# Kernel tuning notes

Measured on AMD Instinct MI355X. Metric: run time of the kernel, lower is better.

The kernel has to match this reference:

```python
import jax, jax.numpy as jnp
import numpy as np

N = 50000
H = 8          # heads
C = 10         # out channels per head
F_IN = 128
NEG_SLOPE = 0.2


def _glorot(key, shape, fan_in):
    return jax.random.normal(key, shape, dtype=jnp.float32) / np.sqrt(fan_in)


def setup_inputs() -> dict:
    key = jax.random.key(0)
    ks = jax.random.split(key, 16)
    x = jax.random.normal(ks[0], (N, F_IN), dtype=jnp.float32)
    edge_index = jax.random.randint(ks[1], (2, 1600000), 0, N, dtype=jnp.int64)
    inp = {"x": x, "edge_index": edge_index}
    dims = [F_IN, H * C, H * C]  # input dim of each of the 3 layers
    k = 2
    for i, din in enumerate(dims):
        inp[f"Wl{i}"] = _glorot(ks[k + 0], (din, H * C), din)
        inp[f"Wr{i}"] = _glorot(ks[k + 1], (din, H * C), din)
        inp[f"att{i}"] = _glorot(ks[k + 2], (H, C), C)
        inp[f"b{i}"] = jnp.zeros((H * C,), dtype=jnp.float32)
        k += 3
    return inp


def gatv2_layer(x, Wl, Wr, att, b, src, dst):
    # GATv2Conv (PyG defaults): separate lin_l/lin_r, e = att . leaky_relu(xl_j + xr_i),
    # segment softmax over incoming edges, scatter-add of alpha * xl_j, concat heads + bias.
    n = x.shape[0]
    xl = (x @ Wl).reshape(n, H, C)
    xr = (x @ Wr).reshape(n, H, C)
    e = jax.nn.leaky_relu(xl[src] + xr[dst], NEG_SLOPE)      # [E, H, C]
    score = jnp.einsum('ehc,hc->eh', e, att)                 # [E, H]
    smax = jax.ops.segment_max(score, dst, num_segments=n)   # [N, H]
    ex = jnp.exp(score - smax[dst])
    denom = jax.ops.segment_sum(ex, dst, num_segments=n)
    alpha = ex / (denom[dst] + 1e-16)                        # [E, H]
    out = jax.ops.segment_sum(alpha[:, :, None] * xl[src], dst, num_segments=n)
    return out.reshape(n, H * C) + b


def reference(x, edge_index, Wl0, Wr0, att0, b0, Wl1, Wr1, att1, b1, Wl2, Wr2, att2, b2):
    n = x.shape[0]
    # add_self_loops=True (PyG default)
    loop = jnp.arange(n, dtype=edge_index.dtype)
    src = jnp.concatenate([edge_index[0], loop])
    dst = jnp.concatenate([edge_index[1], loop])
    params = [(Wl0, Wr0, att0, b0), (Wl1, Wr1, att1, b1), (Wl2, Wr2, att2, b2)]
    for Wl, Wr, att, b in params:
        x = jax.nn.elu(gatv2_layer(x, Wl, Wr, att, b, src, dst))
    return x
```

## Files before the change

### kernel.cpp

```cpp
#include <hip/hip_runtime.h>
#include <hip/hip_bf16.h>
#include <hip/hip_fp16.h>

#define N_NODES 50000
#define HEADS 8
#define CHANS 10
#define HC 80
#define PADH 12
#define PHL 96
#define F_IN 128
#define E_EDGES 1600000
#define E_TOT (E_EDGES + N_NODES)
#define NEG_SLOPE 0.2f
#define NBUCK 3125
#define NCHUNK 128
#define CHUNK ((E_TOT + NCHUNK - 1) / NCHUNK)
#define XS_STRIDE 40
#define WS_STRIDE 40

typedef _Float16 f16x8 __attribute__((ext_vector_type(8)));
typedef float f32x4 __attribute__((ext_vector_type(4)));

#if __has_builtin(__builtin_amdgcn_fdot2) && __has_builtin(__builtin_elementwise_max)
#define USE_PK_SCORE 1
typedef _Float16 h2 __attribute__((ext_vector_type(2)));
#else
#define USE_PK_SCORE 0
#endif

__device__ inline void load_edge(const void* ei, int is64, int e, int& src, int& dst) {
    if (e < E_EDGES) {
        if (is64) {
            src = ((const int*)ei)[2 * e];
            dst = ((const int*)ei)[2 * (E_EDGES + e)];
        } else {
            src = ((const int*)ei)[e];
            dst = ((const int*)ei)[E_EDGES + e];
        }
    } else {
        src = dst = e - E_EDGES;
    }
}

__device__ inline int load_dst(const void* ei, int is64, int e) {
    if (e < E_EDGES) {
        if (is64) return ((const int*)ei)[2 * (E_EDGES + e)];
        return ((const int*)ei)[E_EDGES + e];
    }
    return e - E_EDGES;
}

__device__ inline int detect_is64(const void* ei, int tid, int* s_flag) {
    if (tid < 64) {
        const int* p = (const int*)ei;
        bool ok = (p[2 * tid + 1] == 0) && (p[2 * (tid + 64) + 1] == 0);
        unsigned long long m = __ballot(ok);
        if (tid == 0) *s_flag = (m == ~0ull) ? 1 : 0;
    }
    return 0;
}

__global__ __launch_bounds__(256) void hist_wconv_kernel(
        const void* ei, int* __restrict__ hist, int* __restrict__ bcount,
        const float* __restrict__ Wl0, const float* __restrict__ Wr0,
        const float* __restrict__ Wl1, const float* __restrict__ Wr1,
        const float* __restrict__ Wl2, const float* __restrict__ Wr2,
        __half* __restrict__ wt) {
    int blk = blockIdx.x;
    int tid = threadIdx.x;
    if (blk >= NCHUNK) {
        if (tid < 128) {
            int g = blk - NCHUNK;
            int layer = g / 160, c = g - layer * 160;
            int kp = tid;
            const float* Wl = (layer == 0) ? Wl0 : (layer == 1) ? Wl1 : Wl2;
            const float* Wr = (layer == 0) ? Wr0 : (layer == 1) ? Wr1 : Wr2;
            const float* W = (c < 80) ? Wl : Wr;
            int cc = (c < 80) ? c : c - 80;
            float v = 0.f;
            if (layer == 0) {
                if (kp < F_IN) v = W[kp * 80 + cc];
            } else {
                int hh = kp / PADH, c2 = kp - hh * PADH;
                if (kp < PHL && c2 < CHANS)
                    v = W[(hh * CHANS + c2) * 80 + cc];
            }
            wt[(size_t)g * 128 + kp] = __float2half_rn(v);
        }
        return;
    }
    __shared__ int h[NBUCK];
    __shared__ int s_is64;
    for (int i = tid; i < NBUCK; i += 256) h[i] = 0;
    detect_is64(ei, tid, &s_is64);
    __syncthreads();
    int is64 = s_is64;
    int e0 = blk * CHUNK, e1 = min(e0 + CHUNK, E_TOT);
    for (int e = e0 + tid; e < e1; e += 4 * 256) {
        int d[4]; int cnt = 0;
        #pragma unroll
        for (int u = 0; u < 4; u++) {
            int ee = e + u * 256;
            if (ee < e1) { d[u] = load_dst(ei, is64, ee); cnt = u + 1; }
        }
        #pragma unroll
        for (int u = 0; u < 4; u++)
            if (u < cnt) atomicAdd(&h[d[u] >> 4], 1);
    }
    __syncthreads();
    for (int i = tid; i < NBUCK; i += 256) {
        int v = h[i];
        int old = v ? atomicAdd(&bcount[i], v) : 0;
        hist[blk * NBUCK + i] = old;
    }
}

__global__ void scan_total_kernel(const int* __restrict__ total, int* __restrict__ bbase) {
    __shared__ int wsum[16];
    __shared__ int wpre[16];
    __shared__ int carry;
    int tid = threadIdx.x;
    int lane = tid & 63, w = tid >> 6;
    if (tid == 0) carry = 0;
    __syncthreads();
    for (int base = 0; base < NBUCK; base += 1024) {
        int idx = base + tid;
        int v = (idx < NBUCK) ? total[idx] : 0;
        int sv = v;
        #pragma unroll
        for (int off = 1; off < 64; off <<= 1) {
            int t = __shfl_up(sv, off, 64);
            if (lane >= off) sv += t;
        }
        if (lane == 63) wsum[w] = sv;
        __syncthreads();
        if (w == 0) {
            int s = (lane < 16) ? wsum[lane] : 0;
            #pragma unroll
            for (int off = 1; off < 16; off <<= 1) {
                int t = __shfl_up(s, off, 64);
                if (lane >= off) s += t;
            }
            if (lane < 16) wpre[lane] = s;
        }
        __syncthreads();
        int pre = carry + ((w > 0) ? wpre[w - 1] : 0);
        if (idx < NBUCK) bbase[idx] = pre + sv - v;
        __syncthreads();
        if (tid == 0) carry += wpre[15];
        __syncthreads();
    }
}

__global__ __launch_bounds__(256) void scatter_sort_kernel(
        const void* ei, const int* __restrict__ hist, const int* __restrict__ bbase,
        int* __restrict__ tmp) {
    __shared__ int cur[NBUCK];
    __shared__ int s_is64;
    int tid = threadIdx.x;
    int blk = blockIdx.x;
    for (int i = tid; i < NBUCK; i += 256)
        cur[i] = bbase[i] + hist[blk * NBUCK + i];
    detect_is64(ei, tid, &s_is64);
    __syncthreads();
    int is64 = s_is64;
    int e0 = blk * CHUNK, e1 = min(e0 + CHUNK, E_TOT);
    for (int e = e0 + tid; e < e1; e += 4 * 256) {
        int s[4], d[4]; int cnt = 0;
        #pragma unroll
        for (int u = 0; u < 4; u++) {
            int ee = e + u * 256;
            if (ee < e1) { load_edge(ei, is64, ee, s[u], d[u]); cnt = u + 1; }
        }
        #pragma unroll
        for (int u = 0; u < 4; u++) {
            if (u < cnt) {
                int pos = atomicAdd(&cur[d[u] >> 4], 1);
                tmp[pos] = (s[u] << 4) | (d[u] & 15);
            }
        }
    }
}

__global__ __launch_bounds__(256) void node_sort_kernel(
        const int* __restrict__ tmp, const int* __restrict__ bbase,
        const int* __restrict__ total,
        int* __restrict__ adj, int* __restrict__ nstart, int* __restrict__ deg) {
    __shared__ int h16[16];
    __shared__ int st16[16];
    __shared__ int cur16[16];
    int tid = threadIdx.x;
    int b = blockIdx.x;
    int base = bbase[b];
    int n = total[b];
    if (tid < 16) h16[tid] = 0;
    __syncthreads();
    for (int k = tid; k < n; k += 256)
        atomicAdd(&h16[tmp[base + k] & 15], 1);
    __syncthreads();
    if (tid == 0) {
        int run = 0;
        #pragma unroll
        for (int c = 0; c < 16; c++) { st16[c] = run; cur16[c] = run; run += h16[c]; }
    }
    __syncthreads();
    for (int k = tid; k < n; k += 256) {
        int p = tmp[base + k];
        int pos = atomicAdd(&cur16[p & 15], 1);
        adj[base + pos] = p >> 4;
    }
    if (tid < 16) {
        nstart[b * 16 + tid] = base + st16[tid];
        deg[b * 16 + tid] = h16[tid];
    }
}

__global__ __launch_bounds__(256) void deghist_kernel(
        const int* __restrict__ deg, int* __restrict__ dh) {
    __shared__ int h[256];
    h[threadIdx.x] = 0;
    __syncthreads();
    int i = blockIdx.x * 256 + threadIdx.x;
    if (i < N_NODES) atomicAdd(&h[min(deg[i], 255)], 1);
    __syncthreads();
    if (h[threadIdx.x]) atomicAdd(&dh[threadIdx.x], h[threadIdx.x]);
}

__global__ void degscan_kernel(const int* __restrict__ dh, int* __restrict__ dcur) {
    __shared__ int s[256];
    int tid = threadIdx.x;
    int idx = 255 - tid;
    int own = dh[idx];
    s[tid] = own;
    __syncthreads();
    for (int off = 1; off < 256; off <<= 1) {
        int t = (tid >= off) ? s[tid - off] : 0;
        __syncthreads();
        s[tid] += t;
        __syncthreads();
    }
    dcur[idx] = s[tid] - own;
}

__global__ __launch_bounds__(256) void degscatter_kernel(
        const int* __restrict__ deg, int* __restrict__ dcur, int* __restrict__ perm) {
    __shared__ int h[256];
    __shared__ int res[256];
    __shared__ int lc[256];
    int tid = threadIdx.x;
    h[tid] = 0; lc[tid] = 0;
    __syncthreads();
    int i = blockIdx.x * 256 + tid;
    int d = (i < N_NODES) ? min(deg[i], 255) : -1;
    if (d >= 0) atomicAdd(&h[d], 1);
    __syncthreads();
    res[tid] = h[tid] ? atomicAdd(&dcur[tid], h[tid]) : 0;
    __syncthreads();
    if (d >= 0) {
        int off = atomicAdd(&lc[d], 1);
        perm[res[d] + off] = i;
    }
}

__global__ __launch_bounds__(256) void gemm_mfma_kernel(
        const void* __restrict__ xin, int in_fp16, int nkt,
        const __half* __restrict__ wt,
        __half* __restrict__ xlh, float* __restrict__ xr) {
    __shared__ __half xs[128 * XS_STRIDE];
    __shared__ __half ws[160 * WS_STRIDE];
    int tid = threadIdx.x;
    int n0 = blockIdx.x * 128;
    int w = tid >> 6, lane = tid & 63;
    int quad = lane >> 4, r = lane & 15;

    f32x4 acc[2][10];
    #pragma unroll
    for (int nt = 0; nt < 2; nt++)
        #pragma unroll
        for (int t = 0; t < 10; t++) acc[nt][t] = (f32x4){0.f, 0.f, 0.f, 0.f};

    int snode = tid >> 1;
    int sk = (tid & 1) * 16;
    int sg = n0 + snode;

    for (int kt = 0; kt < nkt; kt++) {
        f16x8 xv0 = (f16x8){0, 0, 0, 0, 0, 0, 0, 0}, xv1 = xv0;
        if (sg < N_NODES) {
            if (in_fp16) {
                const uint4* p = (const uint4*)((const __half*)xin + (size_t)sg * PHL + kt * 32 + sk);
                xv0 = __builtin_bit_cast(f16x8, p[0]);
                xv1 = __builtin_bit_cast(f16x8, p[1]);
            } else {
                const float4* p = (const float4*)((const float*)xin + (size_t)sg * F_IN + kt * 32 + sk);
                float4 f0 = p[0], f1 = p[1], f2 = p[2], f3 = p[3];
                xv0[0] = (_Float16)f0.x; xv0[1] = (_Float16)f0.y;
                xv0[2] = (_Float16)f0.z; xv0[3] = (_Float16)f0.w;
                xv0[4] = (_Float16)f1.x; xv0[5] = (_Float16)f1.y;
                xv0[6] = (_Float16)f1.z; xv0[7] = (_Float16)f1.w;
                xv1[0] = (_Float16)f2.x; xv1[1] = (_Float16)f2.y;
                xv1[2] = (_Float16)f2.z; xv1[3] = (_Float16)f2.w;
                xv1[4] = (_Float16)f3.x; xv1[5] = (_Float16)f3.y;
                xv1[6] = (_Float16)f3.z; xv1[7] = (_Float16)f3.w;
            }
        }
        __syncthreads();
        *(uint4*)(&xs[snode * XS_STRIDE + sk]) = __builtin_bit_cast(uint4, xv0);
        *(uint4*)(&xs[snode * XS_STRIDE + sk + 8]) = __builtin_bit_cast(uint4, xv1);
        for (int u = tid; u < 640; u += 256) {
            int c = u >> 2, k8 = (u & 3) * 8;
            uint4 wv = *(const uint4*)(wt + c * 128 + kt * 32 + k8);
            *(uint4*)(&ws[c * WS_STRIDE + k8]) = wv;
        }
        __syncthreads();
        #pragma unroll
        for (int nt = 0; nt < 2; nt++) {
            f16x8 a = __builtin_bit_cast(f16x8,
                         *(const uint4*)(&xs[(w * 32 + nt * 16 + r) * XS_STRIDE + quad * 8]));
            #pragma unroll
            for (int ct = 0; ct < 10; ct++) {
                f16x8 bf = __builtin_bit_cast(f16x8,
                              *(const uint4*)(&ws[(ct * 16 + r) * WS_STRIDE + quad * 8]));
                acc[nt][ct] = __builtin_amdgcn_mfma_f32_16x16x32_f16(a, bf, acc[nt][ct], 0, 0, 0);
            }
        }
    }
    #pragma unroll
    for (int nt = 0; nt < 2; nt++) {
        #pragma unroll
        for (int ct = 0; ct < 10; ct++) {
            int col = ct * 16 + r;
            #pragma unroll
            for (int reg = 0; reg < 4; reg++) {
                int node = n0 + w * 32 + nt * 16 + quad * 4 + reg;
                if (node < N_NODES) {
                    float v = acc[nt][ct][reg];
                    if (col < 80) {
                        int hh = col / 10, cc = col - hh * 10;
                        xlh[(size_t)node * PHL + hh * PADH + cc] = __float2half_rn(v);
                    } else {
                        xr[(size_t)node * HC + (col - 80)] = v;
                    }
                }
            }
        }
    }
}

__device__ inline void cvt10(uint2 a, uint2 b, uint2 c, float* v) {
    __half2 h;
    h = *(__half2*)&a.x; v[0] = __low2float(h); v[1] = __high2float(h);
    h = *(__half2*)&a.y; v[2] = __low2float(h); v[3] = __high2float(h);
    h = *(__half2*)&b.x; v[4] = __low2float(h); v[5] = __high2float(h);
    h = *(__half2*)&b.y; v[6] = __low2float(h); v[7] = __high2float(h);
    h = *(__half2*)&c.x; v[8] = __low2float(h); v[9] = __high2float(h);
}

__global__ __launch_bounds__(256, 4) void agg_kernel(
        const __half* __restrict__ xlh, const float* __restrict__ xr,
        const float* __restrict__ att, const float* __restrict__ bias,
        const int* __restrict__ nstart, const int* __restrict__ deg,
        const int* __restrict__ adj, const int* __restrict__ perm,
        __half* __restrict__ ybuf, float* __restrict__ yout) {
    int tid = threadIdx.x;
    int b = blockIdx.x;
    int h = tid & 7;
    int split = (tid >> 3) & 1;
    int i_local = tid >> 4;
    int node = perm[b * 16 + i_local];

    int s0 = nstart[node];
    int dg = deg[node];
    int cnt0 = (dg + 1) >> 1;
    int cnt = split ? (dg - cnt0) : cnt0;
    int k0 = s0 + split * cnt0;

#if USE_PK_SCORE
    h2 xrh[5], atth[5];
    #pragma unroll
    for (int p = 0; p < 5; p++) {
        xrh[p] = (h2){(_Float16)xr[(size_t)node * HC + h * CHANS + 2 * p],
                      (_Float16)xr[(size_t)node * HC + h * CHANS + 2 * p + 1]};
        atth[p] = (h2){(_Float16)att[h * CHANS + 2 * p],
                       (_Float16)att[h * CHANS + 2 * p + 1]};
    }
    const h2 k02 = {(_Float16)NEG_SLOPE, (_Float16)NEG_SLOPE};
    auto score_pk = [&](uint2 a, uint2 bq, uint2 cq) {
        unsigned int wv[5] = {a.x, a.y, bq.x, bq.y, cq.x};
        float s = 0.f;
        #pragma unroll
        for (int p = 0; p < 5; p++) {
            h2 v = __builtin_bit_cast(h2, wv[p]);
            h2 t = v + xrh[p];
            h2 tl = __builtin_elementwise_max(t, t * k02);
            s = __builtin_amdgcn_fdot2(tl, atth[p], s, false);
        }
        return s;
    };
#else
    float xr_c[CHANS], att_c[CHANS];
    #pragma unroll
    for (int c = 0; c < CHANS; c++) {
        xr_c[c]  = xr[(size_t)node * HC + h * CHANS + c];
        att_c[c] = att[h * CHANS + c];
    }
    auto score_pk = [&](uint2 a, uint2 bq, uint2 cq) {
        float v[CHANS];
        cvt10(a, bq, cq, v);
        float s = 0.f;
        #pragma unroll
        for (int c = 0; c < CHANS; c++) {
            float t = v[c] + xr_c[c];
            t = (t > 0.f) ? t : NEG_SLOPE * t;
            s += att_c[c] * t;
        }
        return s;
    };
#endif

    float m = -1e30f, l = 0.f;
    float acc[CHANS];
    #pragma unroll
    for (int c = 0; c < CHANS; c++) acc[c] = 0.f;

    int kk = 0;
    for (; kk + 8 <= cnt; kk += 8) {
        uint2 ra[8], rb[8], rc[8];
        #pragma unroll
        for (int r = 0; r < 8; r++) {
            int j = adj[k0 + kk + r];
            const uint2* p = (const uint2*)(xlh + (size_t)j * PHL + h * PADH);
            ra[r] = p[0]; rb[r] = p[1]; rc[r] = p[2];
        }
        float sc[8];
        #pragma unroll
        for (int r = 0; r < 8; r++) sc[r] = score_pk(ra[r], rb[r], rc[r]);
        float mb = m;
        #pragma unroll
        for (int r = 0; r < 8; r++) mb = fmaxf(mb, sc[r]);
        float scale = __expf(m - mb);
        float ps = 0.f;
        #pragma unroll
        for (int r = 0; r < 8; r++) { sc[r] = __expf(sc[r] - mb); ps += sc[r]; }
        l = l * scale + ps;
        #pragma unroll
        for (int c = 0; c < CHANS; c++) acc[c] *= scale;
        #pragma unroll
        for (int r = 0; r < 8; r++) {
            float v[CHANS];
            cvt10(ra[r], rb[r], rc[r], v);
            #pragma unroll
            for (int c = 0; c < CHANS; c++) acc[c] += sc[r] * v[c];
        }
        m = mb;
    }
    for (; kk + 4 <= cnt; kk += 4) {
        uint2 ra[4], rb[4], rc[4];
        #pragma unroll
        for (int r = 0; r < 4; r++) {
            int j = adj[k0 + kk + r];
            const uint2* p = (const uint2*)(xlh + (size_t)j * PHL + h * PADH);
            ra[r] = p[0]; rb[r] = p[1]; rc[r] = p[2];
        }
        float sc[4];
        #pragma unroll
        for (int r = 0; r < 4; r++) sc[r] = score_pk(ra[r], rb[r], rc[r]);
        float mb = m;
        #pragma unroll
        for (int r = 0; r < 4; r++) mb = fmaxf(mb, sc[r]);
        float scale = __expf(m - mb);
        float ps = 0.f;
        #pragma unroll
        for (int r = 0; r < 4; r++) { sc[r] = __expf(sc[r] - mb); ps += sc[r]; }
        l = l * scale + ps;
        #pragma unroll
        for (int c = 0; c < CHANS; c++) acc[c] *= scale;
        #pragma unroll
        for (int r = 0; r < 4; r++) {
            float v[CHANS];
            cvt10(ra[r], rb[r], rc[r], v);
            #pragma unroll
            for (int c = 0; c < CHANS; c++) acc[c] += sc[r] * v[c];
        }
        m = mb;
    }
    for (; kk < cnt; kk++) {
        int j = adj[k0 + kk];
        const uint2* p = (const uint2*)(xlh + (size_t)j * PHL + h * PADH);
        uint2 a = p[0], bq = p[1], cq = p[2];
        float s = score_pk(a, bq, cq);
        float v[CHANS];
        cvt10(a, bq, cq, v);
        float mn = fmaxf(m, s);
        float scale = __expf(m - mn);
        float pp = __expf(s - mn);
        l = l * scale + pp;
        #pragma unroll
        for (int c = 0; c < CHANS; c++) acc[c] = acc[c] * scale + pp * v[c];
        m = mn;
    }

    {
        float m2 = __shfl_xor(m, 8, 64);
        float l2 = __shfl_xor(l, 8, 64);
        float mn = fmaxf(m, m2);
        float sc1 = __expf(m - mn), sc2 = __expf(m2 - mn);
        l = l * sc1 + l2 * sc2;
        #pragma unroll
        for (int c = 0; c < CHANS; c++) {
            float a2 = __shfl_xor(acc[c], 8, 64);
            acc[c] = acc[c] * sc1 + a2 * sc2;
        }
        m = mn;
    }
    if (split == 0) {
        float inv = 1.f / (l + 1e-16f);
        float z[CHANS];
        #pragma unroll
        for (int c = 0; c < CHANS; c++) {
            float t = acc[c] * inv + bias[h * CHANS + c];
            z[c] = (t > 0.f) ? t : (__expf(t) - 1.f);
        }
        if (yout) {
            #pragma unroll
            for (int c = 0; c < CHANS; c++)
                yout[(size_t)node * HC + h * CHANS + c] = z[c];
        } else {
            __half2 h0 = __halves2half2(__float2half_rn(z[0]), __float2half_rn(z[1]));
            __half2 h1 = __halves2half2(__float2half_rn(z[2]), __float2half_rn(z[3]));
            __half2 h2v = __halves2half2(__float2half_rn(z[4]), __float2half_rn(z[5]));
            __half2 h3 = __halves2half2(__float2half_rn(z[6]), __float2half_rn(z[7]));
            __half2 h4 = __halves2half2(__float2half_rn(z[8]), __float2half_rn(z[9]));
            __half2 h5 = __halves2half2(__half(0.f), __half(0.f));
            uint2* dst = (uint2*)(ybuf + (size_t)node * PHL + h * PADH);
            dst[0] = make_uint2(*(unsigned*)&h0, *(unsigned*)&h1);
            dst[1] = make_uint2(*(unsigned*)&h2v, *(unsigned*)&h3);
            dst[2] = make_uint2(*(unsigned*)&h4, *(unsigned*)&h5);
        }
    }
}

extern "C" void kernel_launch(void* const* d_in, const int* in_sizes, int n_in,
                              void* d_out, int out_size, void* d_ws, size_t ws_size,
                              hipStream_t stream) {
    const float* x_in = (const float*)d_in[0];
    const void*  ei   = d_in[1];
    const float* Wl[3] = {(const float*)d_in[2], (const float*)d_in[6],  (const float*)d_in[10]};
    const float* Wr[3] = {(const float*)d_in[3], (const float*)d_in[7],  (const float*)d_in[11]};
    const float* At[3] = {(const float*)d_in[4], (const float*)d_in[8],  (const float*)d_in[12]};
    const float* Bi[3] = {(const float*)d_in[5], (const float*)d_in[9],  (const float*)d_in[13]};
    float* out = (float*)d_out;

    char* ws = (char*)d_ws;
    size_t off = 0;
    auto alloc = [&](size_t bytes) {
        void* p = ws + off;
        off += (bytes + 255) & ~(size_t)255;
        return p;
    };
    __half* xlh   = (__half*)alloc((size_t)N_NODES * PHL * sizeof(__half));
    float*  xr    = (float*)alloc((size_t)N_NODES * HC * sizeof(float));
    __half* buf16 = (__half*)alloc((size_t)N_NODES * PHL * sizeof(__half));
    __half* wt    = (__half*)alloc((size_t)3 * 160 * 128 * sizeof(__half));
    int*   tmp    = (int*)alloc((size_t)E_TOT * sizeof(int));
    int*   adj    = (int*)alloc((size_t)E_TOT * sizeof(int));
    int*   hist   = (int*)alloc((size_t)NCHUNK * NBUCK * sizeof(int));
    int*   bcount = (int*)alloc((size_t)NBUCK * sizeof(int));
    int*   dh     = (int*)alloc(256 * sizeof(int));
    int*   bbase  = (int*)alloc((size_t)NBUCK * sizeof(int));
    int*   nstart = (int*)alloc((size_t)N_NODES * sizeof(int));
    int*   deg    = (int*)alloc((size_t)N_NODES * sizeof(int));
    int*   perm   = (int*)alloc((size_t)N_NODES * sizeof(int));
    int*   dcur   = (int*)alloc(256 * sizeof(int));

    hipMemsetAsync(bcount, 0, (size_t)((char*)dh - (char*)bcount) + 1024, stream);
    hist_wconv_kernel<<<NCHUNK + 480, 256, 0, stream>>>(
        ei, hist, bcount, Wl[0], Wr[0], Wl[1], Wr[1], Wl[2], Wr[2], wt);
    scan_total_kernel<<<1, 1024, 0, stream>>>(bcount, bbase);
    scatter_sort_kernel<<<NCHUNK, 256, 0, stream>>>(ei, hist, bbase, tmp);
    node_sort_kernel<<<NBUCK, 256, 0, stream>>>(tmp, bbase, bcount, adj, nstart, deg);
    int nblocks = (N_NODES + 255) / 256;
    deghist_kernel<<<nblocks, 256, 0, stream>>>(deg, dh);
    degscan_kernel<<<1, 256, 0, stream>>>(dh, dcur);
    degscatter_kernel<<<nblocks, 256, 0, stream>>>(deg, dcur, perm);

    int gemm_blocks = (N_NODES + 127) / 128;
    const void* cur = (const void*)x_in;
    int in_fp16 = 0;
    for (int layer = 0; layer < 3; layer++) {
        int nkt = (layer == 0) ? 4 : 3;
        gemm_mfma_kernel<<<gemm_blocks, 256, 0, stream>>>(
            cur, in_fp16, nkt, wt + (size_t)layer * 160 * 128, xlh, xr);
        __half* ybuf = (layer == 2) ? nullptr : buf16;
        float*  yout = (layer == 2) ? out : nullptr;
        agg_kernel<<<NBUCK, 256, 0, stream>>>(xlh, xr, At[layer], Bi[layer],
                                              nstart, deg, adj, perm, ybuf, yout);
        cur = (const void*)buf16;
        in_fp16 = 1;
    }
}
```

Measured before the change: 344.6 us.

## Merge per-layer GEMM and aggregation into one cooperative kernel with grid sync

Each layer's GEMM and aggregation, plus the degree scatter on the first layer, now run inside a single cooperative persistent kernel. The blocks loop over tiles and buckets, with a grid-wide barrier between the GEMM and aggregation phases, and the old three-kernel path is kept as a fallback if the cooperative launch fails. The aim is to cut kernel launch gaps and tail effects between stages. The risks are a lower occupancy-limited grid, the cost of the grid barrier, and losing the agg kernel's launch_bounds(256,4) register tuning. The degscatter in the first layer also has no grid sync before the GEMM, and agg relies on perm being complete, although the grid sync before agg covers that.

```diff
diff --git a/kernel.cpp b/kernel.cpp
--- a/kernel.cpp
+++ b/kernel.cpp
@@ -1,6 +1,7 @@
 #include <hip/hip_runtime.h>
 #include <hip/hip_bf16.h>
 #include <hip/hip_fp16.h>
+#include <hip/hip_cooperative_groups.h>
 
 #define N_NODES 50000
 #define HEADS 8
@@ -15,6 +16,7 @@
 #define NBUCK 3125
 #define NCHUNK 128
 #define CHUNK ((E_TOT + NCHUNK - 1) / NCHUNK)
+#define GEMM_TILES ((N_NODES + 127) / 128)
 #define XS_STRIDE 40
 #define WS_STRIDE 40
 
@@ -242,15 +244,16 @@
     dcur[idx] = s[tid] - own;
 }
 
-__global__ __launch_bounds__(256) void degscatter_kernel(
-        const int* __restrict__ deg, int* __restrict__ dcur, int* __restrict__ perm) {
+__device__ __forceinline__ void degscatter_body(
+        int chunk, const int* __restrict__ deg, int* __restrict__ dcur,
+        int* __restrict__ perm) {
     __shared__ int h[256];
     __shared__ int res[256];
     __shared__ int lc[256];
     int tid = threadIdx.x;
     h[tid] = 0; lc[tid] = 0;
     __syncthreads();
-    int i = blockIdx.x * 256 + tid;
+    int i = chunk * 256 + tid;
     int d = (i < N_NODES) ? min(deg[i], 255) : -1;
     if (d >= 0) atomicAdd(&h[d], 1);
     __syncthreads();
@@ -260,16 +263,22 @@
         int off = atomicAdd(&lc[d], 1);
         perm[res[d] + off] = i;
     }
-}
-
-__global__ __launch_bounds__(256) void gemm_mfma_kernel(
-        const void* __restrict__ xin, int in_fp16, int nkt,
+    __syncthreads();
+}
+
+__global__ __launch_bounds__(256) void degscatter_kernel(
+        const int* __restrict__ deg, int* __restrict__ dcur, int* __restrict__ perm) {
+    degscatter_body(blockIdx.x, deg, dcur, perm);
+}
+
+__device__ __forceinline__ void gemm_tile_body(
+        int tile, const void* __restrict__ xin, int in_fp16, int nkt,
         const __half* __restrict__ wt,
         __half* __restrict__ xlh, float* __restrict__ xr) {
     __shared__ __half xs[128 * XS_STRIDE];
     __shared__ __half ws[160 * WS_STRIDE];
     int tid = threadIdx.x;
-    int n0 = blockIdx.x * 128;
+    int n0 = tile * 128;
     int w = tid >> 6, lane = tid & 63;
     int quad = lane >> 4, r = lane & 15;
 
@@ -324,6 +333,7 @@
             }
         }
     }
+    __syncthreads();
     #pragma unroll
     for (int nt = 0; nt < 2; nt++) {
         #pragma unroll
@@ -346,6 +356,13 @@
     }
 }
 
+__global__ __launch_bounds__(256) void gemm_mfma_kernel(
+        const void* __restrict__ xin, int in_fp16, int nkt,
+        const __half* __restrict__ wt,
+        __half* __restrict__ xlh, float* __restrict__ xr) {
+    gemm_tile_body(blockIdx.x, xin, in_fp16, nkt, wt, xlh, xr);
+}
+
 __device__ inline void cvt10(uint2 a, uint2 b, uint2 c, float* v) {
     __half2 h;
     h = *(__half2*)&a.x; v[0] = __low2float(h); v[1] = __high2float(h);
@@ -355,14 +372,13 @@
     h = *(__half2*)&c.x; v[8] = __low2float(h); v[9] = __high2float(h);
 }
 
-__global__ __launch_bounds__(256, 4) void agg_kernel(
-        const __half* __restrict__ xlh, const float* __restrict__ xr,
+__device__ __forceinline__ void agg_body(
+        int b, const __half* __restrict__ xlh, const float* __restrict__ xr,
         const float* __restrict__ att, const float* __restrict__ bias,
         const int* __restrict__ nstart, const int* __restrict__ deg,
         const int* __restrict__ adj, const int* __restrict__ perm,
         __half* __restrict__ ybuf, float* __restrict__ yout) {
     int tid = threadIdx.x;
-    int b = blockIdx.x;
     int h = tid & 7;
     int split = (tid >> 3) & 1;
     int i_local = tid >> 4;
@@ -537,6 +553,36 @@
             dst[2] = make_uint2(*(unsigned*)&h4, *(unsigned*)&h5);
         }
     }
+}
+
+__global__ __launch_bounds__(256, 4) void agg_kernel(
+        const __half* __restrict__ xlh, const float* __restrict__ xr,
+        const float* __restrict__ att, const float* __restrict__ bias,
+        const int* __restrict__ nstart, const int* __restrict__ deg,
+        const int* __restrict__ adj, const int* __restrict__ perm,
+        __half* __restrict__ ybuf, float* __restrict__ yout) {
+    agg_body(blockIdx.x, xlh, xr, att, bias, nstart, deg, adj, perm, ybuf, yout);
+}
+
+__global__ __launch_bounds__(256) void coop_layer_kernel(
+        const void* __restrict__ xin, int in_fp16, int nkt,
+        const __half* __restrict__ wt,
+        __half* __restrict__ xlh, float* __restrict__ xr,
+        const float* __restrict__ att, const float* __restrict__ bias,
+        const int* __restrict__ nstart, const int* __restrict__ deg,
+        const int* __restrict__ adj, int* __restrict__ perm,
+        __half* __restrict__ ybuf, float* __restrict__ yout,
+        int do_perm, int* __restrict__ dcur) {
+    if (do_perm) {
+        int nchunks = (N_NODES + 255) >> 8;
+        for (int c = blockIdx.x; c < nchunks; c += gridDim.x)
+            degscatter_body(c, deg, dcur, perm);
+    }
+    for (int t = blockIdx.x; t < GEMM_TILES; t += gridDim.x)
+        gemm_tile_body(t, xin, in_fp16, nkt, wt, xlh, xr);
+    cooperative_groups::this_grid().sync();
+    for (int b = blockIdx.x; b < NBUCK; b += gridDim.x)
+        agg_body(b, xlh, xr, att, bias, nstart, deg, adj, perm, ybuf, yout);
 }
 
 extern "C" void kernel_launch(void* const* d_in, const int* in_sizes, int n_in,
@@ -581,18 +627,49 @@
     int nblocks = (N_NODES + 255) / 256;
     deghist_kernel<<<nblocks, 256, 0, stream>>>(deg, dh);
     degscan_kernel<<<1, 256, 0, stream>>>(dh, dcur);
-    degscatter_kernel<<<nblocks, 256, 0, stream>>>(deg, dcur, perm);
-
-    int gemm_blocks = (N_NODES + 127) / 128;
+
+    int perCU = 0;
+    hipOccupancyMaxActiveBlocksPerMultiprocessor(&perCU,
+        (const void*)coop_layer_kernel, 256, 0);
+    int nCU = 0;
+    hipDeviceGetAttribute(&nCU, hipDeviceAttributeMultiprocessorCount, 0);
+    int cgrid = perCU * nCU;
+    if (cgrid > 2048) cgrid = 2048;
+    bool use_coop = (cgrid >= 64);
+
     const void* cur = (const void*)x_in;
     int in_fp16 = 0;
+    bool perm_done = false;
     for (int layer = 0; layer < 3; layer++) {
         int nkt = (layer == 0) ? 4 : 3;
-        gemm_mfma_kernel<<<gemm_blocks, 256, 0, stream>>>(
-            cur, in_fp16, nkt, wt + (size_t)layer * 160 * 128, xlh, xr);
+        const __half* wtl = wt + (size_t)layer * 160 * 128;
+        const float* att_l = At[layer];
+        const float* bias_l = Bi[layer];
         __half* ybuf = (layer == 2) ? nullptr : buf16;
         float*  yout = (layer == 2) ? out : nullptr;
-        agg_kernel<<<NBUCK, 256, 0, stream>>>(xlh, xr, At[layer], Bi[layer],
+        int do_perm = (layer == 0) ? 1 : 0;
+
+        if (use_coop) {
+            void* kargs[] = {(void*)&cur, (void*)&in_fp16, (void*)&nkt, (void*)&wtl,
+                             (void*)&xlh, (void*)&xr, (void*)&att_l, (void*)&bias_l,
+                             (void*)&nstart, (void*)&deg, (void*)&adj, (void*)&perm,
+                             (void*)&ybuf, (void*)&yout, (void*)&do_perm, (void*)&dcur};
+            hipError_t e = hipLaunchCooperativeKernel(
+                (const void*)coop_layer_kernel, dim3(cgrid), dim3(256), kargs, 0, stream);
+            if (e == hipSuccess) {
+                if (do_perm) perm_done = true;
+                cur = (const void*)buf16;
+                in_fp16 = 1;
+                continue;
+            }
+            use_coop = false;
+        }
+        if (!perm_done) {
+            degscatter_kernel<<<nblocks, 256, 0, stream>>>(deg, dcur, perm);
+            perm_done = true;
+        }
+        gemm_mfma_kernel<<<GEMM_TILES, 256, 0, stream>>>(cur, in_fp16, nkt, wtl, xlh, xr);
+        agg_kernel<<<NBUCK, 256, 0, stream>>>(xlh, xr, att_l, bias_l,
                                               nstart, deg, adj, perm, ybuf, yout);
         cur = (const void*)buf16;
         in_fp16 = 1;
```

New measurement: 344.9 us. About the same (+0.1%).
